# Performance work log

Measured on AMD Instinct MI355X. Metric: run time of the kernel, lower is better.

## Reference

```python
import jax, jax.numpy as jnp
import numpy as np

FACTOR = 1.0
KERNEL = 3
PAD = 1
STRIDE = 1


def setup_inputs() -> dict:
    key = jax.random.key(0)
    ks = jax.random.split(key, 7)
    B_, Cin, Cout, L, CODE = 32, 128, 128, 4096, 2
    return {
        "input": jax.random.normal(ks[0], (B_, Cin, L), dtype=jnp.float32),
        "codes": jax.random.normal(ks[1], (B_, CODE, CODE), dtype=jnp.float32),
        "weight": jax.random.normal(ks[2], (Cout, Cin, KERNEL), dtype=jnp.float32) * 0.05,
        "A": jax.random.normal(ks[3], (Cin, CODE, KERNEL), dtype=jnp.float32) * 0.05,
        "B": jax.random.normal(ks[4], (Cout, CODE, KERNEL), dtype=jnp.float32) * 0.05,
        "bias": jax.random.normal(ks[5], (Cout,), dtype=jnp.float32) * 0.05,
        "bias_context": jax.random.normal(ks[6], (CODE, Cout), dtype=jnp.float32) * 0.05,
    }


def reference(input, codes, weight, A, B, bias, bias_context):
    # Hypernetwork-generated per-sample conv weights (low-rank via codes)
    w = jnp.einsum('ick,bcr->birk', A, codes)            # (b, in, code, k)
    context_w = jnp.einsum('birk,ork->boik', w, B)       # (b, out, in, k)
    combined_weight = weight + FACTOR * context_w        # (b, out, in, k)

    diag = jnp.diagonal(codes, axis1=-2, axis2=-1)       # (b, code)
    context_bias = diag @ bias_context                   # (b, out)
    combined_bias = bias + FACTOR * context_bias         # (b, out)

    # circular padding along spatial axis
    padded = jnp.pad(input, ((0, 0), (0, 0), (PAD, PAD)), mode='wrap')
    L_out = (input.shape[-1] + 2 * PAD - KERNEL) // STRIDE + 1
    # windowed view: (b, in, L_out, k) via k shifted slices (k is tiny, loop ok)
    windows = jnp.stack([padded[:, :, j:j + L_out * STRIDE:STRIDE] for j in range(KERNEL)], axis=-1)
    out = jnp.einsum('bihw,boiw->boh', windows, combined_weight)
    return out + combined_bias[..., None]
```

## Files before the change

kernel.cpp:

```cpp
#include <hip/hip_runtime.h>
#include <hip/hip_bf16.h>
#include <stdint.h>
#include <stddef.h>

#define L_LEN 4096
#define CIN   128
#define COUT  128
#define NB    32
#define KTOT  384
#define TN    64
#define ROWS  (TN + 2)

typedef __bf16 bf16x8 __attribute__((ext_vector_type(8)));
typedef float  f32x4  __attribute__((ext_vector_type(4)));

__device__ __forceinline__ uint16_t f2bf(float f) {
    union { float f; uint32_t u; } v; v.f = f;
    return (uint16_t)((v.u + 0x7fffu + ((v.u >> 16) & 1u)) >> 16);
}
__device__ __forceinline__ uint32_t pack2(float lo, float hi) {
    return (uint32_t)f2bf(lo) | ((uint32_t)f2bf(hi) << 16);
}

__global__ __launch_bounds__(256) void geps_combine(
    const float* __restrict__ codes, const float* __restrict__ weight,
    const float* __restrict__ Amat,  const float* __restrict__ Bmat,
    const float* __restrict__ bias,  const float* __restrict__ bias_ctx,
    uint16_t* __restrict__ Wc, float* __restrict__ cbias)
{
    int tid = blockIdx.x * 256 + threadIdx.x;
    if (tid < NB * COUT * KTOT) {
        int j    = tid & 7;
        int lane = (tid >> 3) & 63;
        int mt   = (tid >> 9) & 1;
        int tmp  = tid >> 10;
        int t    = tmp % 12;
        int bo   = tmp / 12;
        int og   = bo & 3;
        int b    = bo >> 2;
        int col  = t * 32 + (lane >> 4) * 8 + j;
        int k    = col >> 7;
        int i    = col & 127;
        int o    = og * 32 + mt * 16 + (lane & 15);
        float cw = 0.f;
        #pragma unroll
        for (int c = 0; c < 2; ++c) {
            float a = Amat[i * 6 + c * 3 + k];
            #pragma unroll
            for (int r = 0; r < 2; ++r)
                cw += a * codes[b * 4 + c * 2 + r] * Bmat[o * 6 + r * 3 + k];
        }
        float val = weight[o * 384 + i * 3 + k] + cw;
        Wc[tid] = f2bf(val);
    }
    if (tid < NB * COUT) {
        int b = tid >> 7, o = tid & 127;
        float cb = bias[o];
        #pragma unroll
        for (int c = 0; c < 2; ++c)
            cb += codes[b * 4 + c * 2 + c] * bias_ctx[c * 128 + o];
        cbias[tid] = cb;
    }
}


#define LOADQ(C, SB)                                                         \
    {                                                                        \
        int L_p4 = ((C) << 3) + (tid >> 4);                                  \
        int L_qd = tid & 15;                                                 \
        const float* L_r0 = inb + (size_t)(4 * L_p4) * L_LEN + h0 + 4 * L_qd; \
        (SB)[0] = *(const float4*)(L_r0);                                    \
        (SB)[1] = *(const float4*)(L_r0 + L_LEN);                            \
        (SB)[2] = *(const float4*)(L_r0 + 2 * L_LEN);                        \
        (SB)[3] = *(const float4*)(L_r0 + 3 * L_LEN);                        \
    }

#define PACKQ(C, SB)                                                         \
    {                                                                        \
        int P_p4 = ((C) << 3) + (tid >> 4);                                  \
        int P_qd = tid & 15;                                                 \
        const int P_off = (4 * P_p4) & 7;                                    \
        const int P_pc  = P_p4 >> 1;                                         \
        _Pragma("unroll")                                                    \
        for (int P_j4 = 0; P_j4 < 4; ++P_j4) {                               \
            int P_r  = 1 + 4 * P_qd + P_j4;                                  \
            int P_ch = P_pc ^ (P_r & 15);                                    \
            uint2 P_w;                                                       \
            P_w.x = pack2(((const float*)&(SB)[0])[P_j4],                    \
                          ((const float*)&(SB)[1])[P_j4]);                   \
            P_w.y = pack2(((const float*)&(SB)[2])[P_j4],                    \
                          ((const float*)&(SB)[3])[P_j4]);                   \
            *(uint2*)&Xt[P_r * 128 + (P_ch << 3) + P_off] = P_w;             \
        }                                                                    \
    }

__global__ __launch_bounds__(128, 3) void geps_conv(
    const float* __restrict__ in, const uint16_t* __restrict__ Wc,
    const float* __restrict__ cbias, float* __restrict__ out)
{
    __shared__ uint16_t __attribute__((aligned(16))) Xt[ROWS * 128];
    __shared__ float cb[64];

    const int tid  = threadIdx.x;
    const int d    = blockIdx.x;
    const int xcd  = d & 7;
    const int dm   = d >> 3;
    const int og   = dm & 1;
    const int ht   = (dm >> 1) & 63;
    const int b    = 4 * xcd + (dm >> 7);
    const int h0   = ht * TN;
    const int lane = tid & 63;
    const int w    = tid >> 6;
    const int m16  = lane & 15;
    const int q    = lane >> 4;
    const int og32 = og * 2 + w;

    if (tid < 64) cb[tid] = cbias[b * COUT + og * 64 + tid];

    const float* inb = in + (size_t)b * CIN * L_LEN;
    const uint16_t* WcW = Wc + (size_t)(b * 4 + og32) * 12288 + lane * 8;

    float4 st[2][4];
    float  hx0, hx1;
    {
        int L_p    = tid & 63;
        int L_side = tid >> 6;
        int L_r    = L_side ? (ROWS - 1) : 0;
        int L_gh   = (h0 - 1 + L_r) & (L_LEN - 1);
        hx0 = inb[(size_t)(2 * L_p) * L_LEN + L_gh];
        hx1 = inb[(size_t)(2 * L_p + 1) * L_LEN + L_gh];
    }
    LOADQ(0, st[0])
    #pragma unroll
    for (int c = 0; c < 4; ++c) {
        if (c < 3) LOADQ(c + 1, st[(c + 1) & 1])
        asm volatile("" ::: "memory");
        PACKQ(c, st[c & 1])
    }
    {
        int P_p     = tid & 63;
        int P_side  = tid >> 6;
        int P_hr    = P_side ? (ROWS - 1) : 0;
        int P_chunk = (P_p >> 2) ^ (P_hr & 15);
        *(uint32_t*)&Xt[P_hr * 128 + (P_chunk << 3) + ((2 * P_p) & 7)] =
            pack2(hx0, hx1);
    }

    __syncthreads();

    f32x4 acc[2][4];
    #pragma unroll
    for (int a = 0; a < 2; ++a)
        #pragma unroll
        for (int cc = 0; cc < 4; ++cc) acc[a][cc] = 0.0f;

    bf16x8 ar[3][2];
    ar[0][0] = *(const bf16x8*)(WcW);
    ar[0][1] = *(const bf16x8*)(WcW + 512);
    ar[1][0] = *(const bf16x8*)(WcW + 1024);
    ar[1][1] = *(const bf16x8*)(WcW + 1536);

    #pragma unroll
    for (int t = 0; t < 12; ++t) {
        if (t + 2 < 12) {
            ar[(t + 2) % 3][0] = *(const bf16x8*)(WcW + (t + 2) * 1024);
            ar[(t + 2) % 3][1] = *(const bf16x8*)(WcW + (t + 2) * 1024 + 512);
        }
        const int k   = t >> 2;
        const int i0c = (t & 3) << 2;
        bf16x8 bfv[4];
        #pragma unroll
        for (int nt = 0; nt < 4; ++nt) {
            int r  = nt * 16 + m16 + k;
            int ch = (i0c + q) ^ (r & 15);
            bfv[nt] = *(const bf16x8*)&Xt[r * 128 + (ch << 3)];
        }
        #pragma unroll
        for (int nt = 0; nt < 4; ++nt) {
            acc[0][nt] = __builtin_amdgcn_mfma_f32_16x16x32_bf16(
                ar[t % 3][0], bfv[nt], acc[0][nt], 0, 0, 0);
            acc[1][nt] = __builtin_amdgcn_mfma_f32_16x16x32_bf16(
                ar[t % 3][1], bfv[nt], acc[1][nt], 0, 0, 0);
        }
    }

    float* outb = out + (size_t)b * COUT * L_LEN + h0;
    #pragma unroll
    for (int mt = 0; mt < 2; ++mt) {
        #pragma unroll
        for (int reg = 0; reg < 4; ++reg) {
            int o_loc = 32 * w + mt * 16 + q * 4 + reg;
            int o     = og * 64 + o_loc;
            float bv  = cb[o_loc];
            float* orow = outb + (size_t)o * L_LEN;
            #pragma unroll
            for (int nt = 0; nt < 4; ++nt)
                __builtin_nontemporal_store(acc[mt][nt][reg] + bv,
                                            &orow[nt * 16 + m16]);
        }
    }
}

extern "C" void kernel_launch(void* const* d_in, const int* in_sizes, int n_in,
                              void* d_out, int out_size, void* d_ws, size_t ws_size,
                              hipStream_t stream) {
    const float* input    = (const float*)d_in[0];
    const float* codes    = (const float*)d_in[1];
    const float* weight   = (const float*)d_in[2];
    const float* Amat     = (const float*)d_in[3];
    const float* Bmat     = (const float*)d_in[4];
    const float* bias     = (const float*)d_in[5];
    const float* bias_ctx = (const float*)d_in[6];
    float* out = (float*)d_out;

    uint16_t* Wc    = (uint16_t*)d_ws;
    float*    cbias = (float*)((char*)d_ws + (size_t)NB * COUT * KTOT * 2);

    geps_combine<<<dim3((NB * COUT * KTOT) / 256), 256, 0, stream>>>(
        codes, weight, Amat, Bmat, bias, bias_ctx, Wc, cbias);
    geps_conv<<<dim3(NB * (L_LEN / TN) * 2), 128, 0, stream>>>(
        input, Wc, cbias, out);
}
```

Before: 143.1 us.

## Enlarge conv tile to 256 columns with all output channels per block

Each block now covers 256 spatial positions and all 128 output channels with 4 waves, where before it covered 64 positions and half the channels. The input tile is staged once in shared memory and reused across four 64-column subtiles, so the duplicate input loads across the two output-channel halves and the halo overhead both go away. Weights are reloaded from global memory for each subtile. Output stores switch from nontemporal to ordinary stores. The larger shared tile (about 66KB) and fewer blocks reduce occupancy and parallelism.

```diff
diff --git a/kernel.cpp b/kernel.cpp
--- a/kernel.cpp
+++ b/kernel.cpp
@@ -8,7 +8,7 @@
 #define COUT  128
 #define NB    32
 #define KTOT  384
-#define TN    64
+#define TN    256
 #define ROWS  (TN + 2)
 
 typedef __bf16 bf16x8 __attribute__((ext_vector_type(8)));
@@ -64,26 +64,27 @@
 }
 
 
-#define LOADQ(C, SB)                                                         \
+#define LOADC(C, SB)                                                         \
     {                                                                        \
-        int L_p4 = ((C) << 3) + (tid >> 4);                                  \
+        int L_p4 = ((C) >> 2) * 16 + (tid >> 4);                             \
         int L_qd = tid & 15;                                                 \
-        const float* L_r0 = inb + (size_t)(4 * L_p4) * L_LEN + h0 + 4 * L_qd; \
+        const float* L_r0 = inb + (size_t)(4 * L_p4) * L_LEN + h0 +          \
+                            ((C) & 3) * 64 + 4 * L_qd;                       \
         (SB)[0] = *(const float4*)(L_r0);                                    \
         (SB)[1] = *(const float4*)(L_r0 + L_LEN);                            \
         (SB)[2] = *(const float4*)(L_r0 + 2 * L_LEN);                        \
         (SB)[3] = *(const float4*)(L_r0 + 3 * L_LEN);                        \
     }
 
-#define PACKQ(C, SB)                                                         \
+#define PACKC(C, SB)                                                         \
     {                                                                        \
-        int P_p4 = ((C) << 3) + (tid >> 4);                                  \
+        int P_p4 = ((C) >> 2) * 16 + (tid >> 4);                             \
         int P_qd = tid & 15;                                                 \
         const int P_off = (4 * P_p4) & 7;                                    \
         const int P_pc  = P_p4 >> 1;                                         \
         _Pragma("unroll")                                                    \
         for (int P_j4 = 0; P_j4 < 4; ++P_j4) {                               \
-            int P_r  = 1 + 4 * P_qd + P_j4;                                  \
+            int P_r  = 1 + ((C) & 3) * 64 + 4 * P_qd + P_j4;                 \
             int P_ch = P_pc ^ (P_r & 15);                                    \
             uint2 P_w;                                                       \
             P_w.x = pack2(((const float*)&(SB)[0])[P_j4],                    \
@@ -94,50 +95,48 @@
         }                                                                    \
     }
 
-__global__ __launch_bounds__(128, 3) void geps_conv(
+__global__ __launch_bounds__(256, 2) void geps_conv(
     const float* __restrict__ in, const uint16_t* __restrict__ Wc,
     const float* __restrict__ cbias, float* __restrict__ out)
 {
     __shared__ uint16_t __attribute__((aligned(16))) Xt[ROWS * 128];
-    __shared__ float cb[64];
+    __shared__ float cb[COUT];
 
     const int tid  = threadIdx.x;
     const int d    = blockIdx.x;
     const int xcd  = d & 7;
-    const int dm   = d >> 3;
-    const int og   = dm & 1;
-    const int ht   = (dm >> 1) & 63;
-    const int b    = 4 * xcd + (dm >> 7);
-    const int h0   = ht * TN;
+    const int b    = 4 * xcd + ((d >> 3) & 3);
+    const int h0   = (d >> 5) * TN;
     const int lane = tid & 63;
-    const int w    = tid >> 6;
+    const int wid  = tid >> 6;
     const int m16  = lane & 15;
     const int q    = lane >> 4;
-    const int og32 = og * 2 + w;
-
-    if (tid < 64) cb[tid] = cbias[b * COUT + og * 64 + tid];
+    const int mq   = wid * 32;
 
     const float* inb = in + (size_t)b * CIN * L_LEN;
-    const uint16_t* WcW = Wc + (size_t)(b * 4 + og32) * 12288 + lane * 8;
-
-    float4 st[2][4];
-    float  hx0, hx1;
+    const uint16_t* WcW = Wc + (size_t)(b * 4 + wid) * 12288 + lane * 8;
+
+    if (tid < COUT) cb[tid] = cbias[b * COUT + tid];
+
+    float hx0, hx1;
     {
         int L_p    = tid & 63;
-        int L_side = tid >> 6;
+        int L_side = (tid >> 6) & 1;
         int L_r    = L_side ? (ROWS - 1) : 0;
         int L_gh   = (h0 - 1 + L_r) & (L_LEN - 1);
         hx0 = inb[(size_t)(2 * L_p) * L_LEN + L_gh];
         hx1 = inb[(size_t)(2 * L_p + 1) * L_LEN + L_gh];
     }
-    LOADQ(0, st[0])
+
+    float4 st[2][4];
+    LOADC(0, st[0])
     #pragma unroll
-    for (int c = 0; c < 4; ++c) {
-        if (c < 3) LOADQ(c + 1, st[(c + 1) & 1])
+    for (int c = 0; c < 8; ++c) {
+        if (c < 7) LOADC(c + 1, st[(c + 1) & 1])
         asm volatile("" ::: "memory");
-        PACKQ(c, st[c & 1])
-    }
-    {
+        PACKC(c, st[c & 1])
+    }
+    if (tid < 128) {
         int P_p     = tid & 63;
         int P_side  = tid >> 6;
         int P_hr    = P_side ? (ROWS - 1) : 0;
@@ -148,55 +147,56 @@
 
     __syncthreads();
 
-    f32x4 acc[2][4];
-    #pragma unroll
-    for (int a = 0; a < 2; ++a)
-        #pragma unroll
-        for (int cc = 0; cc < 4; ++cc) acc[a][cc] = 0.0f;
-
-    bf16x8 ar[3][2];
-    ar[0][0] = *(const bf16x8*)(WcW);
-    ar[0][1] = *(const bf16x8*)(WcW + 512);
-    ar[1][0] = *(const bf16x8*)(WcW + 1024);
-    ar[1][1] = *(const bf16x8*)(WcW + 1536);
-
-    #pragma unroll
-    for (int t = 0; t < 12; ++t) {
-        if (t + 2 < 12) {
-            ar[(t + 2) % 3][0] = *(const bf16x8*)(WcW + (t + 2) * 1024);
-            ar[(t + 2) % 3][1] = *(const bf16x8*)(WcW + (t + 2) * 1024 + 512);
+    #pragma unroll 1
+    for (int s = 0; s < 4; ++s) {
+        f32x4 acc[2][4];
+        #pragma unroll
+        for (int a = 0; a < 2; ++a)
+            #pragma unroll
+            for (int cc = 0; cc < 4; ++cc) acc[a][cc] = 0.0f;
+
+        bf16x8 ar[3][2];
+        ar[0][0] = *(const bf16x8*)(WcW);
+        ar[0][1] = *(const bf16x8*)(WcW + 512);
+        ar[1][0] = *(const bf16x8*)(WcW + 1024);
+        ar[1][1] = *(const bf16x8*)(WcW + 1536);
+
+        #pragma unroll
+        for (int t = 0; t < 12; ++t) {
+            if (t + 2 < 12) {
+                ar[(t + 2) % 3][0] = *(const bf16x8*)(WcW + (t + 2) * 1024);
+                ar[(t + 2) % 3][1] = *(const bf16x8*)(WcW + (t + 2) * 1024 + 512);
+            }
+            const int k   = t >> 2;
+            const int i0c = (t & 3) << 2;
+            bf16x8 bfv[4];
+            #pragma unroll
+            for (int nt = 0; nt < 4; ++nt) {
+                int r  = s * 64 + nt * 16 + m16 + k;
+                int ch = (i0c + q) ^ (r & 15);
+                bfv[nt] = *(const bf16x8*)&Xt[r * 128 + (ch << 3)];
+            }
+            #pragma unroll
+            for (int nt = 0; nt < 4; ++nt) {
+                acc[0][nt] = __builtin_amdgcn_mfma_f32_16x16x32_bf16(
+                    ar[t % 3][0], bfv[nt], acc[0][nt], 0, 0, 0);
+                acc[1][nt] = __builtin_amdgcn_mfma_f32_16x16x32_bf16(
+                    ar[t % 3][1], bfv[nt], acc[1][nt], 0, 0, 0);
+            }
         }
-        const int k   = t >> 2;
-        const int i0c = (t & 3) << 2;
-        bf16x8 bfv[4];
-        #pragma unroll
-        for (int nt = 0; nt < 4; ++nt) {
-            int r  = nt * 16 + m16 + k;
-            int ch = (i0c + q) ^ (r & 15);
-            bfv[nt] = *(const bf16x8*)&Xt[r * 128 + (ch << 3)];
-        }
-        #pragma unroll
-        for (int nt = 0; nt < 4; ++nt) {
-            acc[0][nt] = __builtin_amdgcn_mfma_f32_16x16x32_bf16(
-                ar[t % 3][0], bfv[nt], acc[0][nt], 0, 0, 0);
-            acc[1][nt] = __builtin_amdgcn_mfma_f32_16x16x32_bf16(
-                ar[t % 3][1], bfv[nt], acc[1][nt], 0, 0, 0);
-        }
-    }
-
-    float* outb = out + (size_t)b * COUT * L_LEN + h0;
-    #pragma unroll
-    for (int mt = 0; mt < 2; ++mt) {
-        #pragma unroll
-        for (int reg = 0; reg < 4; ++reg) {
-            int o_loc = 32 * w + mt * 16 + q * 4 + reg;
-            int o     = og * 64 + o_loc;
-            float bv  = cb[o_loc];
-            float* orow = outb + (size_t)o * L_LEN;
-            #pragma unroll
-            for (int nt = 0; nt < 4; ++nt)
-                __builtin_nontemporal_store(acc[mt][nt][reg] + bv,
-                                            &orow[nt * 16 + m16]);
+
+        float* outb = out + (size_t)b * COUT * L_LEN + h0 + s * 64;
+        #pragma unroll
+        for (int mt = 0; mt < 2; ++mt) {
+            #pragma unroll
+            for (int reg = 0; reg < 4; ++reg) {
+                int o = mq + mt * 16 + q * 4 + reg;
+                float bv = cb[o];
+                float* orow = outb + (size_t)o * L_LEN;
+                #pragma unroll
+                for (int nt = 0; nt < 4; ++nt)
+                    orow[nt * 16 + m16] = acc[mt][nt][reg] + bv;
+            }
         }
     }
 }
@@ -218,6 +218,6 @@
 
     geps_combine<<<dim3((NB * COUT * KTOT) / 256), 256, 0, stream>>>(
         codes, weight, Amat, Bmat, bias, bias_ctx, Wc, cbias);
-    geps_conv<<<dim3(NB * (L_LEN / TN) * 2), 128, 0, stream>>>(
+    geps_conv<<<dim3(NB * (L_LEN / TN)), 256, 0, stream>>>(
         input, Wc, cbias, out);
 }
```

Measured after the change: 128.3 us. 10.3% less time.
